# Optimization experiments

Hardware: AMD Instinct MI355X
Metric: run time of the kernel (lower is better)

The kernel has to match this reference:

```python
import jax, jax.numpy as jnp
import numpy as np

ROBOT_ACT, DIRECTION, RESOURCE, REPEAT = 6, 5, 5, 2
EMB, Q = 64, 20
NEG_SLOPE = 0.01  # nn.LeakyReLU default


def setup_inputs() -> dict:
    key = jax.random.key(0)
    ks = jax.random.split(key, 16)
    B, H, W = 16, 48, 48
    inp = {
        "unit_indicator": jax.random.randint(ks[0], (B, H, W), 0, 2).astype(bool),
        "act_type": jax.random.randint(ks[1], (B, H, W, Q), 0, ROBOT_ACT).astype(jnp.int32),
        "direction": jax.random.randint(ks[2], (B, H, W, Q), 0, DIRECTION).astype(jnp.int32),
        "resource": jax.random.randint(ks[3], (B, H, W, Q), 0, RESOURCE).astype(jnp.int32),
        "repeat": jax.random.randint(ks[4], (B, H, W, Q), 0, REPEAT).astype(jnp.int32),
        "amount": jax.random.uniform(ks[5], (B, H, W, Q), jnp.float32),
        "n": jax.random.uniform(ks[6], (B, H, W, Q), jnp.float32),
        # learned params
        "type_table": jax.random.normal(ks[7], (ROBOT_ACT, EMB), jnp.float32),
        "direction_table": jax.random.normal(ks[8], (DIRECTION, EMB), jnp.float32),
        "resource_table": jax.random.normal(ks[9], (RESOURCE, EMB), jnp.float32),
        "repeat_table": jax.random.normal(ks[10], (REPEAT, EMB), jnp.float32),
        "w1": jax.random.normal(ks[11], (Q,), jnp.float32) / np.sqrt(Q),   # Conv3d(1,1,(Q,1,1)) weight
        "b1": jax.random.normal(ks[12], (1,), jnp.float32) * 0.1,
        "w2": jax.random.normal(ks[13], (6,), jnp.float32) / np.sqrt(6.0),  # Conv3d(1,1,(1,1,6)) weight
        "b2": jax.random.normal(ks[14], (1,), jnp.float32) * 0.1,
    }
    return inp


def reference(unit_indicator, act_type, direction, resource, repeat, amount, n,
              type_table, direction_table, resource_table, repeat_table,
              w1, b1, w2, b2):
    # Stack order along the size-6 conv axis: [type, direction, resource, amount, repeat, n].
    # Both conv3ds are linear, so out = LeakyReLU(sum_f w2[f] * (sum_q w1[q]*feat[q,f]) + b1*sum(w2) + b2).
    rep_idx = (repeat != 0).astype(jnp.int32)
    # Per-table: gather [B,H,W,Q,E], contract Q with w1 -> [B,H,W,E]
    c = (w2[0] * jnp.einsum('q,bhwqe->bhwe', w1, type_table[act_type])
         + w2[1] * jnp.einsum('q,bhwqe->bhwe', w1, direction_table[direction])
         + w2[2] * jnp.einsum('q,bhwqe->bhwe', w1, resource_table[resource])
         + w2[4] * jnp.einsum('q,bhwqe->bhwe', w1, repeat_table[rep_idx])
         + (w2[3] * jnp.einsum('q,bhwq->bhw', w1, amount))[..., None]
         + (w2[5] * jnp.einsum('q,bhwq->bhw', w1, n))[..., None]
         + b1 * jnp.sum(w2) + b2)
    out = jnp.where(c >= 0, c, NEG_SLOPE * c)
    out = out * unit_indicator[..., None].astype(out.dtype)  # zeros where no unit
    return jnp.transpose(out, (0, 3, 1, 2))  # [B, E, H, W]
```

## Files before the change

### kernel.cpp

```cpp
#include <hip/hip_runtime.h>

constexpr int Q    = 20;
constexpr int EMB  = 64;
constexpr int Bsz  = 16, H = 48, W = 48;
constexpr int HW   = H * W;
constexpr int NPIX = Bsz * HW;
constexpr int BLOCK = 256;
constexpr int TPP   = 4;
constexpr int PIXPB = BLOCK / TPP;
constexpr int NBLK  = NPIX / PIXPB;

__global__ __launch_bounds__(BLOCK)
void act_pre_kernel(const int* __restrict__ unit,
                    const int* __restrict__ atp,  const int* __restrict__ dirp,
                    const int* __restrict__ resp, const int* __restrict__ repp,
                    const float* __restrict__ amtp, const float* __restrict__ np_,
                    const float* __restrict__ Ttab, const float* __restrict__ Dtab,
                    const float* __restrict__ Rtab, const float* __restrict__ Ptab,
                    const float* __restrict__ w1p,  const float* __restrict__ b1p,
                    const float* __restrict__ w2p,  const float* __restrict__ b2p,
                    float* __restrict__ out)
{
    __shared__ float sc[18][EMB];
    __shared__ float sw1[Q];
    __shared__ float sconst[4];

    const int tid = threadIdx.x;
    for (int i = tid; i < 18 * EMB; i += BLOCK) {
        const int row = i >> 6, e = i & 63;
        float v, s;
        if (row < 6)       { v = Ttab[row * EMB + e];        s = w2p[0]; }
        else if (row < 11) { v = Dtab[(row - 6) * EMB + e];  s = w2p[1]; }
        else if (row < 16) { v = Rtab[(row - 11) * EMB + e]; s = w2p[2]; }
        else               { v = Ptab[(row - 16) * EMB + e]; s = w2p[4]; }
        sc[row][e] = v * s;
    }
    if (tid < Q) sw1[tid] = w1p[tid];
    if (tid == 0) {
        sconst[0] = w2p[3];
        sconst[1] = w2p[5];
        const float sumw2 = w2p[0] + w2p[1] + w2p[2] + w2p[3] + w2p[4] + w2p[5];
        sconst[2] = b1p[0] * sumw2 + b2p[0];
        float sw = 0.f;
        for (int q = 0; q < Q; ++q) sw += w1p[q];
        sconst[3] = sw;
    }
    __syncthreads();

    const int pIB = tid >> 2;
    const int t   = tid & 3;
    const int pix = blockIdx.x * PIXPB + pIB;

    const int base = pix * Q + t * 4;
    const int4   av = *reinterpret_cast<const int4*>(atp  + base);
    const int4   dv = *reinterpret_cast<const int4*>(dirp + base);
    const int4   rv = *reinterpret_cast<const int4*>(resp + base);
    const int4   pv = *reinterpret_cast<const int4*>(repp + base);
    const float4 mv = *reinterpret_cast<const float4*>(amtp + base);
    const float4 nv = *reinterpret_cast<const float4*>(np_  + base);
    const int tail  = pix * Q + 16 + t;
    const int   as = atp[tail],  ds = dirp[tail], rs = resp[tail], ps = repp[tail];
    const float ms = amtp[tail], ns = np_[tail];

    const int   ai[5] = {av.x, av.y, av.z, av.w, as};
    const int   di[5] = {dv.x, dv.y, dv.z, dv.w, ds};
    const int   ri[5] = {rv.x, rv.y, rv.z, rv.w, rs};
    const int   pi[5] = {pv.x, pv.y, pv.z, pv.w, ps};
    const float mf[5] = {mv.x, mv.y, mv.z, mv.w, ms};
    const float nf[5] = {nv.x, nv.y, nv.z, nv.w, ns};

    float cT[6] = {}, cD[5] = {}, cR[5] = {};
    float repAcc = 0.f, amtAcc = 0.f, nAcc = 0.f;

    #pragma unroll
    for (int j = 0; j < 5; ++j) {
        const int q = (j < 4) ? (t * 4 + j) : (16 + t);
        const float wq = sw1[q];
        #pragma unroll
        for (int k = 0; k < 6; ++k) cT[k] += (ai[j] == k) ? wq : 0.f;
        #pragma unroll
        for (int k = 0; k < 5; ++k) cD[k] += (di[j] == k) ? wq : 0.f;
        #pragma unroll
        for (int k = 0; k < 5; ++k) cR[k] += (ri[j] == k) ? wq : 0.f;
        repAcc += (pi[j] != 0) ? wq : 0.f;
        amtAcc += wq * mf[j];
        nAcc   += wq * nf[j];
    }

    #define RED4(x) { x += __shfl_xor(x, 1); x += __shfl_xor(x, 2); }
    #pragma unroll
    for (int k = 0; k < 6; ++k) RED4(cT[k]);
    #pragma unroll
    for (int k = 0; k < 5; ++k) RED4(cD[k]);
    #pragma unroll
    for (int k = 0; k < 5; ++k) RED4(cR[k]);
    RED4(repAcc); RED4(amtAcc); RED4(nAcc);
    #undef RED4

    const float scalar = sconst[0] * amtAcc + sconst[1] * nAcc + sconst[2];
    const float ind = (unit[pix] != 0) ? 1.f : 0.f;

    float coef[18];
    #pragma unroll
    for (int k = 0; k < 6; ++k) coef[k] = cT[k];
    #pragma unroll
    for (int k = 0; k < 5; ++k) coef[6 + k] = cD[k];
    #pragma unroll
    for (int k = 0; k < 5; ++k) coef[11 + k] = cR[k];
    coef[16] = sconst[3] - repAcc;
    coef[17] = repAcc;

    const int b  = pix / HW;
    const int hw = pix - b * HW;
    float* outp = out + b * (EMB * HW) + hw;

    #pragma unroll
    for (int i = 0; i < 4; ++i) {
        const int e0 = t * 16 + i * 4;
        float va0 = scalar, va1 = scalar, va2 = scalar, va3 = scalar;
        #pragma unroll
        for (int k = 0; k < 18; ++k) {
            const float4 sv = *reinterpret_cast<const float4*>(&sc[k][e0]);
            va0 += coef[k] * sv.x;
            va1 += coef[k] * sv.y;
            va2 += coef[k] * sv.z;
            va3 += coef[k] * sv.w;
        }
        va0 = ((va0 >= 0.f) ? va0 : 0.01f * va0) * ind;
        va1 = ((va1 >= 0.f) ? va1 : 0.01f * va1) * ind;
        va2 = ((va2 >= 0.f) ? va2 : 0.01f * va2) * ind;
        va3 = ((va3 >= 0.f) ? va3 : 0.01f * va3) * ind;
        outp[(e0 + 0) * HW] = va0;
        outp[(e0 + 1) * HW] = va1;
        outp[(e0 + 2) * HW] = va2;
        outp[(e0 + 3) * HW] = va3;
    }
}

extern "C" void kernel_launch(void* const* d_in, const int* in_sizes, int n_in,
                              void* d_out, int out_size, void* d_ws, size_t ws_size,
                              hipStream_t stream) {
    const int*   unit = (const int*)  d_in[0];
    const int*   atp  = (const int*)  d_in[1];
    const int*   dirp = (const int*)  d_in[2];
    const int*   resp = (const int*)  d_in[3];
    const int*   repp = (const int*)  d_in[4];
    const float* amtp = (const float*)d_in[5];
    const float* np_  = (const float*)d_in[6];
    const float* Ttab = (const float*)d_in[7];
    const float* Dtab = (const float*)d_in[8];
    const float* Rtab = (const float*)d_in[9];
    const float* Ptab = (const float*)d_in[10];
    const float* w1p  = (const float*)d_in[11];
    const float* b1p  = (const float*)d_in[12];
    const float* w2p  = (const float*)d_in[13];
    const float* b2p  = (const float*)d_in[14];
    float* out = (float*)d_out;

    act_pre_kernel<<<NBLK, BLOCK, 0, stream>>>(
        unit, atp, dirp, resp, repp, amtp, np_,
        Ttab, Dtab, Rtab, Ptab, w1p, b1p, w2p, b2p, out);
}
```

Measured before the change: 14.25 us.

## Eliminate one row per embedding table and use eight threads per pixel

The one-hot counts of each table sum to sum(w1), so the last row of each table is subtracted out and folded into a precomputed per-embedding bias row. This cuts the shared coefficient table from 18 rows to 15 and the per-output FMA count from 18 to 14. Threads per pixel go from 4 to 8, so each thread writes 8 embeddings instead of 16, and only 5 of the 8 threads load the Q inputs, dropping the scalar tail loads. The cost is an extra shuffle stage in the reductions, three idle lanes during loading, and twice as many blocks, each of which recomputes the shared table.

```diff
diff --git a/kernel.cpp b/kernel.cpp
--- a/kernel.cpp
+++ b/kernel.cpp
@@ -6,7 +6,7 @@
 constexpr int HW   = H * W;
 constexpr int NPIX = Bsz * HW;
 constexpr int BLOCK = 256;
-constexpr int TPP   = 4;
+constexpr int TPP   = 8;
 constexpr int PIXPB = BLOCK / TPP;
 constexpr int NBLK  = NPIX / PIXPB;
 
@@ -21,19 +21,26 @@
                     const float* __restrict__ w2p,  const float* __restrict__ b2p,
                     float* __restrict__ out)
 {
-    __shared__ float sc[18][EMB];
+    __shared__ float sc[15][EMB];
     __shared__ float sw1[Q];
-    __shared__ float sconst[4];
+    __shared__ float sconst[3];
 
     const int tid = threadIdx.x;
-    for (int i = tid; i < 18 * EMB; i += BLOCK) {
+    for (int i = tid; i < 15 * EMB; i += BLOCK) {
         const int row = i >> 6, e = i & 63;
-        float v, s;
-        if (row < 6)       { v = Ttab[row * EMB + e];        s = w2p[0]; }
-        else if (row < 11) { v = Dtab[(row - 6) * EMB + e];  s = w2p[1]; }
-        else if (row < 16) { v = Rtab[(row - 11) * EMB + e]; s = w2p[2]; }
-        else               { v = Ptab[(row - 16) * EMB + e]; s = w2p[4]; }
-        sc[row][e] = v * s;
+        float v;
+        if (row < 5)       v = w2p[0] * (Ttab[row * EMB + e]       - Ttab[5 * EMB + e]);
+        else if (row < 9)  v = w2p[1] * (Dtab[(row - 5) * EMB + e] - Dtab[4 * EMB + e]);
+        else if (row < 13) v = w2p[2] * (Rtab[(row - 9) * EMB + e] - Rtab[4 * EMB + e]);
+        else if (row == 13) v = w2p[4] * (Ptab[EMB + e] - Ptab[e]);
+        else {
+            float sumw = 0.f;
+            #pragma unroll
+            for (int q = 0; q < Q; ++q) sumw += w1p[q];
+            v = sumw * (w2p[0] * Ttab[5 * EMB + e] + w2p[1] * Dtab[4 * EMB + e]
+                      + w2p[2] * Rtab[4 * EMB + e] + w2p[4] * Ptab[e]);
+        }
+        sc[row][e] = v;
     }
     if (tid < Q) sw1[tid] = w1p[tid];
     if (tid == 0) {
@@ -41,85 +48,79 @@
         sconst[1] = w2p[5];
         const float sumw2 = w2p[0] + w2p[1] + w2p[2] + w2p[3] + w2p[4] + w2p[5];
         sconst[2] = b1p[0] * sumw2 + b2p[0];
-        float sw = 0.f;
-        for (int q = 0; q < Q; ++q) sw += w1p[q];
-        sconst[3] = sw;
     }
     __syncthreads();
 
-    const int pIB = tid >> 2;
-    const int t   = tid & 3;
+    const int pIB = tid >> 3;
+    const int t   = tid & 7;
     const int pix = blockIdx.x * PIXPB + pIB;
 
-    const int base = pix * Q + t * 4;
-    const int4   av = *reinterpret_cast<const int4*>(atp  + base);
-    const int4   dv = *reinterpret_cast<const int4*>(dirp + base);
-    const int4   rv = *reinterpret_cast<const int4*>(resp + base);
-    const int4   pv = *reinterpret_cast<const int4*>(repp + base);
-    const float4 mv = *reinterpret_cast<const float4*>(amtp + base);
-    const float4 nv = *reinterpret_cast<const float4*>(np_  + base);
-    const int tail  = pix * Q + 16 + t;
-    const int   as = atp[tail],  ds = dirp[tail], rs = resp[tail], ps = repp[tail];
-    const float ms = amtp[tail], ns = np_[tail];
+    float cT[5] = {}, cD[4] = {}, cR[4] = {};
+    float rep = 0.f, amtAcc = 0.f, nAcc = 0.f;
 
-    const int   ai[5] = {av.x, av.y, av.z, av.w, as};
-    const int   di[5] = {dv.x, dv.y, dv.z, dv.w, ds};
-    const int   ri[5] = {rv.x, rv.y, rv.z, rv.w, rs};
-    const int   pi[5] = {pv.x, pv.y, pv.z, pv.w, ps};
-    const float mf[5] = {mv.x, mv.y, mv.z, mv.w, ms};
-    const float nf[5] = {nv.x, nv.y, nv.z, nv.w, ns};
-
-    float cT[6] = {}, cD[5] = {}, cR[5] = {};
-    float repAcc = 0.f, amtAcc = 0.f, nAcc = 0.f;
-
-    #pragma unroll
-    for (int j = 0; j < 5; ++j) {
-        const int q = (j < 4) ? (t * 4 + j) : (16 + t);
-        const float wq = sw1[q];
+    if (t < 5) {
+        const int base = pix * Q + t * 4;
+        const int4   av = *reinterpret_cast<const int4*>(atp  + base);
+        const int4   dv = *reinterpret_cast<const int4*>(dirp + base);
+        const int4   rv = *reinterpret_cast<const int4*>(resp + base);
+        const int4   pv = *reinterpret_cast<const int4*>(repp + base);
+        const float4 mv = *reinterpret_cast<const float4*>(amtp + base);
+        const float4 nv = *reinterpret_cast<const float4*>(np_  + base);
+        const int   ai[4] = {av.x, av.y, av.z, av.w};
+        const int   di[4] = {dv.x, dv.y, dv.z, dv.w};
+        const int   ri[4] = {rv.x, rv.y, rv.z, rv.w};
+        const int   pi[4] = {pv.x, pv.y, pv.z, pv.w};
+        const float mf[4] = {mv.x, mv.y, mv.z, mv.w};
+        const float nf[4] = {nv.x, nv.y, nv.z, nv.w};
         #pragma unroll
-        for (int k = 0; k < 6; ++k) cT[k] += (ai[j] == k) ? wq : 0.f;
-        #pragma unroll
-        for (int k = 0; k < 5; ++k) cD[k] += (di[j] == k) ? wq : 0.f;
-        #pragma unroll
-        for (int k = 0; k < 5; ++k) cR[k] += (ri[j] == k) ? wq : 0.f;
-        repAcc += (pi[j] != 0) ? wq : 0.f;
-        amtAcc += wq * mf[j];
-        nAcc   += wq * nf[j];
+        for (int j = 0; j < 4; ++j) {
+            const float wq = sw1[t * 4 + j];
+            #pragma unroll
+            for (int k = 0; k < 5; ++k) cT[k] += (ai[j] == k) ? wq : 0.f;
+            #pragma unroll
+            for (int k = 0; k < 4; ++k) cD[k] += (di[j] == k) ? wq : 0.f;
+            #pragma unroll
+            for (int k = 0; k < 4; ++k) cR[k] += (ri[j] == k) ? wq : 0.f;
+            rep    += (pi[j] != 0) ? wq : 0.f;
+            amtAcc += wq * mf[j];
+            nAcc   += wq * nf[j];
+        }
     }
 
-    #define RED4(x) { x += __shfl_xor(x, 1); x += __shfl_xor(x, 2); }
+    #define RED8(x) { x += __shfl_xor(x, 1); x += __shfl_xor(x, 2); x += __shfl_xor(x, 4); }
     #pragma unroll
-    for (int k = 0; k < 6; ++k) RED4(cT[k]);
+    for (int k = 0; k < 5; ++k) RED8(cT[k]);
     #pragma unroll
-    for (int k = 0; k < 5; ++k) RED4(cD[k]);
+    for (int k = 0; k < 4; ++k) RED8(cD[k]);
     #pragma unroll
-    for (int k = 0; k < 5; ++k) RED4(cR[k]);
-    RED4(repAcc); RED4(amtAcc); RED4(nAcc);
-    #undef RED4
+    for (int k = 0; k < 4; ++k) RED8(cR[k]);
+    RED8(rep); RED8(amtAcc); RED8(nAcc);
+    #undef RED8
 
     const float scalar = sconst[0] * amtAcc + sconst[1] * nAcc + sconst[2];
     const float ind = (unit[pix] != 0) ? 1.f : 0.f;
 
-    float coef[18];
+    float coef[14];
     #pragma unroll
-    for (int k = 0; k < 6; ++k) coef[k] = cT[k];
+    for (int k = 0; k < 5; ++k) coef[k] = cT[k];
     #pragma unroll
-    for (int k = 0; k < 5; ++k) coef[6 + k] = cD[k];
+    for (int k = 0; k < 4; ++k) coef[5 + k] = cD[k];
     #pragma unroll
-    for (int k = 0; k < 5; ++k) coef[11 + k] = cR[k];
-    coef[16] = sconst[3] - repAcc;
-    coef[17] = repAcc;
+    for (int k = 0; k < 4; ++k) coef[9 + k] = cR[k];
+    coef[13] = rep;
 
     const int b  = pix / HW;
     const int hw = pix - b * HW;
     float* outp = out + b * (EMB * HW) + hw;
 
     #pragma unroll
-    for (int i = 0; i < 4; ++i) {
-        const int e0 = t * 16 + i * 4;
-        float va0 = scalar, va1 = scalar, va2 = scalar, va3 = scalar;
+    for (int i = 0; i < 2; ++i) {
+        const int e0 = t * 8 + i * 4;
+        const float4 bv = *reinterpret_cast<const float4*>(&sc[14][e0]);
+        float va0 = scalar + bv.x, va1 = scalar + bv.y;
+        float va2 = scalar + bv.z, va3 = scalar + bv.w;
         #pragma unroll
-        for (int k = 0; k < 18; ++k) {
+        for (int k = 0; k < 14; ++k) {
             const float4 sv = *reinterpret_cast<const float4*>(&sc[k][e0]);
             va0 += coef[k] * sv.x;
             va1 += coef[k] * sv.y;
```

After: 15.05 us. +5.6%, slower.
